# Optimization experiments

Hardware: AMD Instinct MI355X
Metric: run time of the kernel (lower is better)

## Reference

```python
import jax, jax.numpy as jnp
import numpy as np
import math

B, H, L, D = 2, 16, 2048, 128

def setup_inputs() -> dict:
    key = jax.random.key(0)
    kq, kk, kv, km = jax.random.split(key, 4)
    q = jax.random.normal(kq, (B, H, L, D), dtype=jnp.float32)
    k = jax.random.normal(kk, (B, H, L, D), dtype=jnp.float32)
    v = jax.random.normal(kv, (B, H, L, D), dtype=jnp.float32)
    mask = jax.random.randint(km, (B, 1, L, L), 0, 2, dtype=jnp.int32)
    return {"q": q, "k": k, "v": v, "mask": mask}

def reference(q, k, v, mask):
    d_tensor = q.shape[-1]
    # ReLU applied to V before attention (the custom twist)
    v = jax.nn.relu(v)
    # score = q @ k^T / sqrt(d)  -> [B,H,L,L]
    score = jnp.einsum('bhqd,bhkd->bhqk', q, k) / math.sqrt(d_tensor)
    score = jnp.where(mask == 0, jnp.float32(-10000.0), score)
    attn = jax.nn.softmax(score, axis=-1)
    # result = attn @ relu(v) -> [B,H,L,D]
    return jnp.einsum('bhqk,bhkd->bhqd', attn, v)
```

## Files before the change

kernel.cpp:

```cpp
#include <hip/hip_runtime.h>
#include <hip/hip_bf16.h>
#include <math.h>

typedef __attribute__((ext_vector_type(8)))  short short8;
typedef __attribute__((ext_vector_type(16))) float f32x16;

#define Bc    2
#define Hc    16
#define Lc    2048
#define Dc    128
#define QBLK  128
#define KBLK  64
#define LOG2E 1.4426950408889634f
#define SCALE 0.08838834764831845f
#define SCL2  (SCALE * LOG2E)

#define KB_OFF   0u
#define KB_BYTES (32u * 2048u * 128u * 2u)
#define VT_OFF   (KB_OFF + KB_BYTES)
#define VT_BYTES (32u * 2048u * 128u * 2u)
#define MB_OFF   (VT_OFF + VT_BYTES)

__device__ __forceinline__ unsigned pk2(float a, float b) {
    unsigned short ua = __builtin_bit_cast(unsigned short, __float2bfloat16(a));
    unsigned short ub = __builtin_bit_cast(unsigned short, __float2bfloat16(b));
    return (unsigned)ua | ((unsigned)ub << 16);
}
__device__ __forceinline__ unsigned short bf16b(float a) {
    return __builtin_bit_cast(unsigned short, __float2bfloat16(a));
}
__device__ __forceinline__ void gload_lds16(const void* g, void* l) {
    __builtin_amdgcn_global_load_lds(
        (const __attribute__((address_space(1))) unsigned int*)g,
        (__attribute__((address_space(3))) unsigned int*)l, 16, 0, 0);
}
__device__ __forceinline__ unsigned cvtpk(float lo, float hi) {
    unsigned r;
    asm("v_cvt_pk_bf16_f32 %0, %1, %2" : "=v"(r) : "v"(lo), "v"(hi));
    return r;
}

__global__ void conv_k_kernel(const float* __restrict__ k, unsigned short* __restrict__ kb) {
    int idx8 = blockIdx.x * 256 + threadIdx.x;
    size_t base = (size_t)idx8 * 8;
    float4 f0 = *(const float4*)(k + base);
    float4 f1 = *(const float4*)(k + base + 4);
    uint4 w;
    w.x = pk2(f0.x, f0.y); w.y = pk2(f0.z, f0.w);
    w.z = pk2(f1.x, f1.y); w.w = pk2(f1.z, f1.w);
    *(uint4*)(kb + base) = w;
}

__global__ void transp_v_kernel(const float* __restrict__ v, unsigned short* __restrict__ vt) {
    __shared__ float t[32][33];
    int d0 = blockIdx.x * 32;
    int l0 = blockIdx.y * 32;
    int bh = blockIdx.z;
    int tx = threadIdx.x, ty = threadIdx.y;
    const float* src = v + (size_t)bh * Lc * Dc;
    unsigned short* dst = vt + (size_t)bh * Dc * Lc;
    #pragma unroll
    for (int i = 0; i < 4; ++i) {
        int row = ty * 4 + i;
        t[row][tx] = fmaxf(src[(size_t)(l0 + row) * Dc + d0 + tx], 0.f);
    }
    __syncthreads();
    #pragma unroll
    for (int i = 0; i < 4; ++i) {
        int drow = ty * 4 + i;
        dst[(size_t)(d0 + drow) * Lc + l0 + tx] = bf16b(t[tx][drow]);
    }
}

__global__ void mask_pack_kernel(const int* __restrict__ mask, unsigned long long* __restrict__ mb) {
    int tid  = threadIdx.x;
    int wv   = blockIdx.x * 4 + (tid >> 6);
    int lane = tid & 63;
    int b    = wv >> 16;
    int l    = (wv >> 5) & 2047;
    int ktw  = wv & 31;
    int m = mask[(((size_t)(b * 2048 + l)) << 11) + ktw * 64 + lane];
    unsigned long long bal = __ballot(m != 0);
    if (lane == 0) mb[(((size_t)(b * 32 + ktw)) << 11) + l] = bal;
}

__global__ __launch_bounds__(256, 2) void rev_attn_kernel(
    const float* __restrict__ q,
    const unsigned short* __restrict__ kb,
    const unsigned short* __restrict__ vt,
    const unsigned long long* __restrict__ mb,
    float* __restrict__ out)
{
    __shared__ __align__(16) char smem[65536];

    const int tid  = threadIdx.x;
    const int w    = tid >> 6;
    const int lane = tid & 63;
    const int l31  = lane & 31;
    const int hi   = lane >> 5;
    const int bh   = blockIdx.y;
    const int b    = bh >> 4;
    const int qb   = blockIdx.x * QBLK + w * 32;
    const int qrow = qb + l31;

    const float*              qp = q  + (size_t)bh * Lc * Dc;
    const unsigned short*     kp = kb + (size_t)bh * Lc * Dc;
    const unsigned short*     vp = vt + (size_t)bh * Dc * Lc;
    const unsigned long long* mp = mb + ((size_t)b << 16);
    float*                    op = out + (size_t)bh * Lc * Dc;

    short8 qf[8];
    {
        const float* qr0 = qp + (size_t)qrow * Dc + hi * 8;
        #pragma unroll
        for (int c = 0; c < 8; ++c) {
            const float* src = qr0 + c * 16;
            #pragma unroll
            for (int j = 0; j < 8; ++j)
                qf[c][j] = (short)bf16b(src[j] * SCL2);
        }
    }

    f32x16 o0 = (f32x16)0.f, o1 = (f32x16)0.f, o2 = (f32x16)0.f, o3 = (f32x16)0.f;
    f32x16 lacc = (f32x16)0.f;
    short8 ones;
    #pragma unroll
    for (int j = 0; j < 8; ++j) ones[j] = (short)0x3F80;

    #define STAGE(buf, kt_) do {                                                   \
        char* Kdst = smem + (buf) * 16384;                                         \
        char* Vdst = smem + 32768 + (buf) * 16384;                                 \
        _Pragma("unroll")                                                          \
        for (int p = 0; p < 4; ++p) {                                              \
            int l   = p * 256 + tid;                                               \
            int row = l >> 4, cl = l & 15;                                         \
            int s_  = cl ^ (row & 15);                                             \
            gload_lds16(kp + (size_t)((kt_) + row) * Dc + s_ * 8, Kdst + l * 16);  \
            int ds_ = row + ((s_ >> 3) << 6);                                      \
            int ko_ = (s_ & 7) * 8;                                                \
            gload_lds16(vp + (size_t)ds_ * Lc + (kt_) + ko_, Vdst + l * 16);       \
        }                                                                          \
    } while (0)

    int cur = 0;
    STAGE(0, 0);
    __syncthreads();

    for (int kt = 0; kt < Lc; kt += KBLK) {
        if (kt + KBLK < Lc) STAGE(cur ^ 1, kt + KBLK);
        unsigned long long mw = mp[((size_t)(kt >> 6) << 11) + qrow];
        const char* Kb = smem + cur * 16384;
        const char* Vb = smem + 32768 + cur * 16384;

        f32x16 s0 = (f32x16)0.f, s1 = (f32x16)0.f;
        __builtin_amdgcn_s_setprio(1);
        #pragma unroll
        for (int c = 0; c < 8; ++c) {
            int r0 = l31;
            short8 kf0 = *(const short8*)(Kb + r0 * 256 + ((((c << 1) | hi)) ^ (r0 & 15)) * 16);
            s0 = __builtin_amdgcn_mfma_f32_32x32x16_bf16(kf0, qf[c], s0, 0, 0, 0);
            int r1 = 32 + l31;
            short8 kf1 = *(const short8*)(Kb + r1 * 256 + ((((c << 1) | hi)) ^ (r1 & 15)) * 16);
            s1 = __builtin_amdgcn_mfma_f32_32x32x16_bf16(kf1, qf[c], s1, 0, 0, 0);
        }
        __builtin_amdgcn_s_setprio(0);

        unsigned m0 = ((unsigned)(mw & 0xffffffffull)) >> (4 * hi);
        unsigned m1 = ((unsigned)(mw >> 32)) >> (4 * hi);
        #pragma unroll
        for (int r = 0; r < 16; ++r) {
            const int cs = (r & 3) + 8 * (r >> 2);
            float e0 = exp2f(s0[r]);
            float e1 = exp2f(s1[r]);
            s0[r] = ((m0 >> cs) & 1u) ? e0 : 0.f;
            s1[r] = ((m1 >> cs) & 1u) ? e1 : 0.f;
        }

        short8 pa[4];
        {
            union { unsigned u[4]; short8 v; } t0, t1, t2, t3;
            unsigned a, a2, bb, b2;
            a  = cvtpk(s0[0], s0[1]);  a2 = cvtpk(s0[2], s0[3]);
            bb = cvtpk(s0[4], s0[5]);  b2 = cvtpk(s0[6], s0[7]);
            asm volatile("v_permlane32_swap_b32 %0, %1" : "+v"(a),  "+v"(bb));
            asm volatile("v_permlane32_swap_b32 %0, %1" : "+v"(a2), "+v"(b2));
            t0.u[0] = a; t0.u[1] = a2; t0.u[2] = bb; t0.u[3] = b2;
            a  = cvtpk(s0[8],  s0[9]);  a2 = cvtpk(s0[10], s0[11]);
            bb = cvtpk(s0[12], s0[13]); b2 = cvtpk(s0[14], s0[15]);
            asm volatile("v_permlane32_swap_b32 %0, %1" : "+v"(a),  "+v"(bb));
            asm volatile("v_permlane32_swap_b32 %0, %1" : "+v"(a2), "+v"(b2));
            t1.u[0] = a; t1.u[1] = a2; t1.u[2] = bb; t1.u[3] = b2;
            a  = cvtpk(s1[0], s1[1]);  a2 = cvtpk(s1[2], s1[3]);
            bb = cvtpk(s1[4], s1[5]);  b2 = cvtpk(s1[6], s1[7]);
            asm volatile("v_permlane32_swap_b32 %0, %1" : "+v"(a),  "+v"(bb));
            asm volatile("v_permlane32_swap_b32 %0, %1" : "+v"(a2), "+v"(b2));
            t2.u[0] = a; t2.u[1] = a2; t2.u[2] = bb; t2.u[3] = b2;
            a  = cvtpk(s1[8],  s1[9]);  a2 = cvtpk(s1[10], s1[11]);
            bb = cvtpk(s1[12], s1[13]); b2 = cvtpk(s1[14], s1[15]);
            asm volatile("v_permlane32_swap_b32 %0, %1" : "+v"(a),  "+v"(bb));
            asm volatile("v_permlane32_swap_b32 %0, %1" : "+v"(a2), "+v"(b2));
            t3.u[0] = a; t3.u[1] = a2; t3.u[2] = bb; t3.u[3] = b2;
            pa[0] = t0.v; pa[1] = t1.v; pa[2] = t2.v; pa[3] = t3.v;
        }

        __builtin_amdgcn_s_setprio(1);
        #pragma unroll
        for (int ks = 0; ks < 4; ++ks)
            lacc = __builtin_amdgcn_mfma_f32_32x32x16_bf16(ones, pa[ks], lacc, 0, 0, 0);
        #pragma unroll
        for (int dt = 0; dt < 4; ++dt) {
            int vrow = (dt & 1) * 32 + l31;
            int hs   = dt >> 1;
            int vswz = vrow & 15;
            f32x16 acc = (dt == 0) ? o0 : (dt == 1) ? o1 : (dt == 2) ? o2 : o3;
            #pragma unroll
            for (int ks = 0; ks < 4; ++ks) {
                int off = vrow * 256 + (((hs << 3) | (ks << 1) | hi) ^ vswz) * 16;
                short8 vf = *(const short8*)(Vb + off);
                acc = __builtin_amdgcn_mfma_f32_32x32x16_bf16(vf, pa[ks], acc, 0, 0, 0);
            }
            if (dt == 0) o0 = acc; else if (dt == 1) o1 = acc; else if (dt == 2) o2 = acc; else o3 = acc;
        }
        __builtin_amdgcn_s_setprio(0);

        __syncthreads();
        cur ^= 1;
    }

    __syncthreads();
    float inv = 1.0f / lacc[0];
    float* scr = (float*)(smem + w * 4608);
    const int qq = lane >> 1;
    const int dh = (lane & 1) * 16;
    #pragma unroll
    for (int dt = 0; dt < 4; ++dt) {
        const f32x16& oo = (dt == 0) ? o0 : (dt == 1) ? o1 : (dt == 2) ? o2 : o3;
        #pragma unroll
        for (int r = 0; r < 16; ++r) {
            int drow = (r & 3) + 8 * (r >> 2) + 4 * hi;
            scr[drow * 36 + l31] = oo[r] * inv;
        }
        asm volatile("s_waitcnt lgkmcnt(0)" ::: "memory");
        __builtin_amdgcn_sched_barrier(0);
        float t[16];
        #pragma unroll
        for (int c2 = 0; c2 < 16; ++c2)
            t[c2] = scr[(dh + c2) * 36 + qq];
        asm volatile("s_waitcnt lgkmcnt(0)" ::: "memory");
        __builtin_amdgcn_sched_barrier(0);
        float* od = op + (size_t)(qb + qq) * Dc + dt * 32 + dh;
        #pragma unroll
        for (int c2 = 0; c2 < 4; ++c2) {
            float4 f4; f4.x = t[c2*4]; f4.y = t[c2*4+1]; f4.z = t[c2*4+2]; f4.w = t[c2*4+3];
            *(float4*)(od + c2 * 4) = f4;
        }
    }
}

extern "C" void kernel_launch(void* const* d_in, const int* in_sizes, int n_in,
                              void* d_out, int out_size, void* d_ws, size_t ws_size,
                              hipStream_t stream) {
    const float* q    = (const float*)d_in[0];
    const float* k    = (const float*)d_in[1];
    const float* v    = (const float*)d_in[2];
    const int*   mask = (const int*)d_in[3];
    float*       out  = (float*)d_out;

    char* ws = (char*)d_ws;
    unsigned short*     kb  = (unsigned short*)(ws + KB_OFF);
    unsigned short*     vt  = (unsigned short*)(ws + VT_OFF);
    unsigned long long* mbp = (unsigned long long*)(ws + MB_OFF);

    hipLaunchKernelGGL(conv_k_kernel, dim3(4096), dim3(256), 0, stream, k, kb);
    hipLaunchKernelGGL(transp_v_kernel, dim3(4, 64, 32), dim3(32, 8), 0, stream, v, vt);
    hipLaunchKernelGGL(mask_pack_kernel, dim3(32768), dim3(256), 0, stream, mask, mbp);

    hipLaunchKernelGGL(rev_attn_kernel, dim3(Lc / QBLK, Bc * Hc), dim3(256), 0, stream,
                       q, kb, vt, mbp, out);
}
```

Before: 130.9 us.

## Merge prepass kernels and interleave softmax slices with PV MFMAs under manual barriers

Folds the K conversion, V relu-transpose and mask packing into one launch, with each mask-packing wave handling 16 rows. In the attention loop, the next tile's prefetch always runs (wrapping on the last iteration). __syncthreads is replaced by an s_waitcnt vmcnt(9) plus s_barrier, which lets the next tile's loads stay in flight. The exp/mask/pack step is split into four slices, each feeding its PV MFMAs right away, to overlap VALU work with matrix work and lower register pressure. The cost is a redundant final prefetch and fragile hand-counted waitcnts.

```diff
diff --git a/kernel.cpp b/kernel.cpp
--- a/kernel.cpp
+++ b/kernel.cpp
@@ -40,48 +40,51 @@
     return r;
 }
 
-__global__ void conv_k_kernel(const float* __restrict__ k, unsigned short* __restrict__ kb) {
-    int idx8 = blockIdx.x * 256 + threadIdx.x;
-    size_t base = (size_t)idx8 * 8;
-    float4 f0 = *(const float4*)(k + base);
-    float4 f1 = *(const float4*)(k + base + 4);
-    uint4 w;
-    w.x = pk2(f0.x, f0.y); w.y = pk2(f0.z, f0.w);
-    w.z = pk2(f1.x, f1.y); w.w = pk2(f1.z, f1.w);
-    *(uint4*)(kb + base) = w;
-}
-
-__global__ void transp_v_kernel(const float* __restrict__ v, unsigned short* __restrict__ vt) {
+__global__ void prepass_kernel(const float* __restrict__ k, const float* __restrict__ v,
+                               const int* __restrict__ mask,
+                               unsigned short* __restrict__ kb, unsigned short* __restrict__ vt,
+                               unsigned long long* __restrict__ mb) {
     __shared__ float t[32][33];
-    int d0 = blockIdx.x * 32;
-    int l0 = blockIdx.y * 32;
-    int bh = blockIdx.z;
-    int tx = threadIdx.x, ty = threadIdx.y;
-    const float* src = v + (size_t)bh * Lc * Dc;
-    unsigned short* dst = vt + (size_t)bh * Dc * Lc;
-    #pragma unroll
-    for (int i = 0; i < 4; ++i) {
-        int row = ty * 4 + i;
-        t[row][tx] = fmaxf(src[(size_t)(l0 + row) * Dc + d0 + tx], 0.f);
-    }
-    __syncthreads();
-    #pragma unroll
-    for (int i = 0; i < 4; ++i) {
-        int drow = ty * 4 + i;
-        dst[(size_t)(d0 + drow) * Lc + l0 + tx] = bf16b(t[tx][drow]);
-    }
-}
-
-__global__ void mask_pack_kernel(const int* __restrict__ mask, unsigned long long* __restrict__ mb) {
-    int tid  = threadIdx.x;
-    int wv   = blockIdx.x * 4 + (tid >> 6);
-    int lane = tid & 63;
-    int b    = wv >> 16;
-    int l    = (wv >> 5) & 2047;
-    int ktw  = wv & 31;
-    int m = mask[(((size_t)(b * 2048 + l)) << 11) + ktw * 64 + lane];
-    unsigned long long bal = __ballot(m != 0);
-    if (lane == 0) mb[(((size_t)(b * 32 + ktw)) << 11) + l] = bal;
+    int bid = blockIdx.x;
+    int tid = threadIdx.x;
+    if (bid < 4096) {
+        size_t base = ((size_t)bid * 256 + tid) * 8;
+        float4 f0 = *(const float4*)(k + base);
+        float4 f1 = *(const float4*)(k + base + 4);
+        uint4 w;
+        w.x = pk2(f0.x, f0.y); w.y = pk2(f0.z, f0.w);
+        w.z = pk2(f1.x, f1.y); w.w = pk2(f1.z, f1.w);
+        *(uint4*)(kb + base) = w;
+    } else if (bid < 12288) {
+        int b2 = bid - 4096;
+        int bh = b2 >> 8, rem = b2 & 255;
+        int l0 = (rem >> 2) * 32, d0 = (rem & 3) * 32;
+        int tx = tid & 31, ty = tid >> 5;
+        const float* src = v + (size_t)bh * Lc * Dc;
+        unsigned short* dst = vt + (size_t)bh * Dc * Lc;
+        #pragma unroll
+        for (int i = 0; i < 4; ++i) {
+            int row = ty * 4 + i;
+            t[row][tx] = fmaxf(src[(size_t)(l0 + row) * Dc + d0 + tx], 0.f);
+        }
+        __syncthreads();
+        #pragma unroll
+        for (int i = 0; i < 4; ++i) {
+            int drow = ty * 4 + i;
+            dst[(size_t)(d0 + drow) * Lc + l0 + tx] = bf16b(t[tx][drow]);
+        }
+    } else {
+        int m = bid - 12288;
+        int wv = tid >> 6, lane = tid & 63;
+        #pragma unroll
+        for (int i = 0; i < 16; ++i) {
+            int wid = m * 64 + wv * 16 + i;
+            int b = wid >> 16, l = (wid >> 5) & 2047, ktw = wid & 31;
+            int mm = mask[(((size_t)(b * 2048 + l)) << 11) + ktw * 64 + lane];
+            unsigned long long bal = __ballot(mm != 0);
+            if (lane == 0) mb[(((size_t)(b * 32 + ktw)) << 11) + l] = bal;
+        }
+    }
 }
 
 __global__ __launch_bounds__(256, 2) void rev_attn_kernel(
@@ -142,13 +145,56 @@
         }                                                                          \
     } while (0)
 
+    #define MK_SLICE(PA, SV, J0, CS0, MREG) do {                                   \
+        float e0 = ((MREG >> (CS0 + 0)) & 1u)  ? exp2f(SV[J0 + 0]) : 0.f;          \
+        float e1 = ((MREG >> (CS0 + 1)) & 1u)  ? exp2f(SV[J0 + 1]) : 0.f;          \
+        float e2 = ((MREG >> (CS0 + 2)) & 1u)  ? exp2f(SV[J0 + 2]) : 0.f;          \
+        float e3 = ((MREG >> (CS0 + 3)) & 1u)  ? exp2f(SV[J0 + 3]) : 0.f;          \
+        float e4 = ((MREG >> (CS0 + 8)) & 1u)  ? exp2f(SV[J0 + 4]) : 0.f;          \
+        float e5 = ((MREG >> (CS0 + 9)) & 1u)  ? exp2f(SV[J0 + 5]) : 0.f;          \
+        float e6 = ((MREG >> (CS0 + 10)) & 1u) ? exp2f(SV[J0 + 6]) : 0.f;          \
+        float e7 = ((MREG >> (CS0 + 11)) & 1u) ? exp2f(SV[J0 + 7]) : 0.f;          \
+        unsigned a_ = cvtpk(e0, e1), a2_ = cvtpk(e2, e3);                          \
+        unsigned b_ = cvtpk(e4, e5), b2_ = cvtpk(e6, e7);                          \
+        asm volatile("v_permlane32_swap_b32 %0, %1" : "+v"(a_),  "+v"(b_));        \
+        asm volatile("v_permlane32_swap_b32 %0, %1" : "+v"(a2_), "+v"(b2_));       \
+        union { unsigned u[4]; short8 v8; } tu_;                                   \
+        tu_.u[0] = a_; tu_.u[1] = a2_; tu_.u[2] = b_; tu_.u[3] = b2_;              \
+        PA = tu_.v8;                                                               \
+    } while (0)
+
+    #define PV_SLICE(PA, KS) do {                                                  \
+        __builtin_amdgcn_s_setprio(1);                                             \
+        lacc = __builtin_amdgcn_mfma_f32_32x32x16_bf16(ones, PA, lacc, 0, 0, 0);   \
+        short8 vfa = *(const short8*)(Vb + vrowA * 256 + ((((0 << 3) | ((KS) << 1) | hi) ^ vswz) * 16)); \
+        o0 = __builtin_amdgcn_mfma_f32_32x32x16_bf16(vfa, PA, o0, 0, 0, 0);        \
+        short8 vfb = *(const short8*)(Vb + vrowB * 256 + ((((0 << 3) | ((KS) << 1) | hi) ^ vswz) * 16)); \
+        o1 = __builtin_amdgcn_mfma_f32_32x32x16_bf16(vfb, PA, o1, 0, 0, 0);        \
+        short8 vfc = *(const short8*)(Vb + vrowA * 256 + ((((1 << 3) | ((KS) << 1) | hi) ^ vswz) * 16)); \
+        o2 = __builtin_amdgcn_mfma_f32_32x32x16_bf16(vfc, PA, o2, 0, 0, 0);        \
+        short8 vfd = *(const short8*)(Vb + vrowB * 256 + ((((1 << 3) | ((KS) << 1) | hi) ^ vswz) * 16)); \
+        o3 = __builtin_amdgcn_mfma_f32_32x32x16_bf16(vfd, PA, o3, 0, 0, 0);        \
+        __builtin_amdgcn_s_setprio(0);                                             \
+    } while (0)
+
+    const int vrowA = l31;
+    const int vrowB = 32 + l31;
+    const int vswz  = l31 & 15;
+
     int cur = 0;
     STAGE(0, 0);
-    __syncthreads();
+    asm volatile("s_waitcnt vmcnt(0)" ::: "memory");
+    __builtin_amdgcn_s_barrier();
+    __builtin_amdgcn_sched_barrier(0);
 
     for (int kt = 0; kt < Lc; kt += KBLK) {
-        if (kt + KBLK < Lc) STAGE(cur ^ 1, kt + KBLK);
+        STAGE(cur ^ 1, (kt + KBLK) & (Lc - 1));
         unsigned long long mw = mp[((size_t)(kt >> 6) << 11) + qrow];
+
+        asm volatile("s_waitcnt vmcnt(9)" ::: "memory");
+        __builtin_amdgcn_s_barrier();
+        __builtin_amdgcn_sched_barrier(0);
+
         const char* Kb = smem + cur * 16384;
         const char* Vb = smem + 32768 + cur * 16384;
 
@@ -167,63 +213,16 @@
 
         unsigned m0 = ((unsigned)(mw & 0xffffffffull)) >> (4 * hi);
         unsigned m1 = ((unsigned)(mw >> 32)) >> (4 * hi);
-        #pragma unroll
-        for (int r = 0; r < 16; ++r) {
-            const int cs = (r & 3) + 8 * (r >> 2);
-            float e0 = exp2f(s0[r]);
-            float e1 = exp2f(s1[r]);
-            s0[r] = ((m0 >> cs) & 1u) ? e0 : 0.f;
-            s1[r] = ((m1 >> cs) & 1u) ? e1 : 0.f;
-        }
-
-        short8 pa[4];
-        {
-            union { unsigned u[4]; short8 v; } t0, t1, t2, t3;
-            unsigned a, a2, bb, b2;
-            a  = cvtpk(s0[0], s0[1]);  a2 = cvtpk(s0[2], s0[3]);
-            bb = cvtpk(s0[4], s0[5]);  b2 = cvtpk(s0[6], s0[7]);
-            asm volatile("v_permlane32_swap_b32 %0, %1" : "+v"(a),  "+v"(bb));
-            asm volatile("v_permlane32_swap_b32 %0, %1" : "+v"(a2), "+v"(b2));
-            t0.u[0] = a; t0.u[1] = a2; t0.u[2] = bb; t0.u[3] = b2;
-            a  = cvtpk(s0[8],  s0[9]);  a2 = cvtpk(s0[10], s0[11]);
-            bb = cvtpk(s0[12], s0[13]); b2 = cvtpk(s0[14], s0[15]);
-            asm volatile("v_permlane32_swap_b32 %0, %1" : "+v"(a),  "+v"(bb));
-            asm volatile("v_permlane32_swap_b32 %0, %1" : "+v"(a2), "+v"(b2));
-            t1.u[0] = a; t1.u[1] = a2; t1.u[2] = bb; t1.u[3] = b2;
-            a  = cvtpk(s1[0], s1[1]);  a2 = cvtpk(s1[2], s1[3]);
-            bb = cvtpk(s1[4], s1[5]);  b2 = cvtpk(s1[6], s1[7]);
-            asm volatile("v_permlane32_swap_b32 %0, %1" : "+v"(a),  "+v"(bb));
-            asm volatile("v_permlane32_swap_b32 %0, %1" : "+v"(a2), "+v"(b2));
-            t2.u[0] = a; t2.u[1] = a2; t2.u[2] = bb; t2.u[3] = b2;
-            a  = cvtpk(s1[8],  s1[9]);  a2 = cvtpk(s1[10], s1[11]);
-            bb = cvtpk(s1[12], s1[13]); b2 = cvtpk(s1[14], s1[15]);
-            asm volatile("v_permlane32_swap_b32 %0, %1" : "+v"(a),  "+v"(bb));
-            asm volatile("v_permlane32_swap_b32 %0, %1" : "+v"(a2), "+v"(b2));
-            t3.u[0] = a; t3.u[1] = a2; t3.u[2] = bb; t3.u[3] = b2;
-            pa[0] = t0.v; pa[1] = t1.v; pa[2] = t2.v; pa[3] = t3.v;
-        }
-
-        __builtin_amdgcn_s_setprio(1);
-        #pragma unroll
-        for (int ks = 0; ks < 4; ++ks)
-            lacc = __builtin_amdgcn_mfma_f32_32x32x16_bf16(ones, pa[ks], lacc, 0, 0, 0);
-        #pragma unroll
-        for (int dt = 0; dt < 4; ++dt) {
-            int vrow = (dt & 1) * 32 + l31;
-            int hs   = dt >> 1;
-            int vswz = vrow & 15;
-            f32x16 acc = (dt == 0) ? o0 : (dt == 1) ? o1 : (dt == 2) ? o2 : o3;
-            #pragma unroll
-            for (int ks = 0; ks < 4; ++ks) {
-                int off = vrow * 256 + (((hs << 3) | (ks << 1) | hi) ^ vswz) * 16;
-                short8 vf = *(const short8*)(Vb + off);
-                acc = __builtin_amdgcn_mfma_f32_32x32x16_bf16(vf, pa[ks], acc, 0, 0, 0);
-            }
-            if (dt == 0) o0 = acc; else if (dt == 1) o1 = acc; else if (dt == 2) o2 = acc; else o3 = acc;
-        }
-        __builtin_amdgcn_s_setprio(0);
-
-        __syncthreads();
+
+        short8 pa;
+        MK_SLICE(pa, s0, 0, 0,  m0);  PV_SLICE(pa, 0);
+        MK_SLICE(pa, s0, 8, 16, m0);  PV_SLICE(pa, 1);
+        MK_SLICE(pa, s1, 0, 0,  m1);  PV_SLICE(pa, 2);
+        MK_SLICE(pa, s1, 8, 16, m1);  PV_SLICE(pa, 3);
+
+        asm volatile("" ::: "memory");
+        __builtin_amdgcn_s_barrier();
+        __builtin_amdgcn_sched_barrier(0);
         cur ^= 1;
     }
 
@@ -271,10 +270,7 @@
     unsigned short*     vt  = (unsigned short*)(ws + VT_OFF);
     unsigned long long* mbp = (unsigned long long*)(ws + MB_OFF);
 
-    hipLaunchKernelGGL(conv_k_kernel, dim3(4096), dim3(256), 0, stream, k, kb);
-    hipLaunchKernelGGL(transp_v_kernel, dim3(4, 64, 32), dim3(32, 8), 0, stream, v, vt);
-    hipLaunchKernelGGL(mask_pack_kernel, dim3(32768), dim3(256), 0, stream, mask, mbp);
-
+    hipLaunchKernelGGL(prepass_kernel, dim3(14336), dim3(256), 0, stream, k, v, mask, kb, vt, mbp);
     hipLaunchKernelGGL(rev_attn_kernel, dim3(Lc / QBLK, Bc * Hc), dim3(256), 0, stream,
                        q, kb, vt, mbp, out);
 }
```

Result: faster. 123.3 us (-5.8%).
